# Kernel optimization log

Hardware: AMD Instinct MI355X
Metric: run time of the kernel (lower is better)

Reference implementation:

```python
import jax, jax.numpy as jnp
import numpy as np

LN_EPS = 1e-5

def setup_inputs() -> dict:
    num_nodes, embed_dim, bs, E = 10000, 64, 32, 200000
    key = jax.random.key(0)
    ks = jax.random.split(key, 8)
    d_in = 2 * embed_dim + 1  # msg_dim = 1
    d_h = 4 * embed_dim
    return {
        "users": jax.random.randint(ks[0], (E,), 0, num_nodes * bs),
        "items": jax.random.randint(ks[1], (E,), 0, num_nodes * bs),
        "messages": jax.random.normal(ks[2], (E,), dtype=jnp.float32),
        "bs": bs,
        "user_emb": jax.random.normal(ks[3], (num_nodes, embed_dim), dtype=jnp.float32) * 0.02,
        "item_emb": jax.random.normal(ks[4], (num_nodes, embed_dim), dtype=jnp.float32) * 0.02,
        "W1": jax.random.normal(ks[5], (d_in, d_h), dtype=jnp.float32) * 0.02,
        "b1": jnp.zeros((d_h,), dtype=jnp.float32),
        "ln_g": jnp.ones((d_h,), dtype=jnp.float32),
        "ln_b": jnp.zeros((d_h,), dtype=jnp.float32),
        "W2": jax.random.normal(ks[6], (d_h, d_h), dtype=jnp.float32) * 0.02,
        "b2": jnp.zeros((d_h,), dtype=jnp.float32),
    }

def reference(users, items, messages, bs, user_emb, item_emb, W1, b1, ln_g, ln_b, W2, b2):
    num_nodes, embed_dim = user_emb.shape
    N = num_nodes * bs
    msgs = messages.astype(jnp.float32).reshape(-1, 1)          # [E,1]
    ue = user_emb[users % num_nodes]                             # [E,D]
    ie = item_emb[items % num_nodes]                             # [E,D]
    x = jnp.concatenate([ue, ie, msgs], axis=-1)                 # [E,2D+1]
    h = x @ W1 + b1                                              # [E,4D]
    mu = jnp.mean(h, axis=-1, keepdims=True)
    var = jnp.mean(jnp.square(h - mu), axis=-1, keepdims=True)
    hn = (h - mu) * jax.lax.rsqrt(var + LN_EPS) * ln_g + ln_b
    enc = hn @ W2 + b2                                           # [E,4D]
    uu, iu, ug, ig = jnp.split(enc, 4, axis=-1)                  # each [E,D]
    user_state = jnp.zeros((N, embed_dim), jnp.float32).at[users].add(uu)
    item_state = jnp.zeros((N, embed_dim), jnp.float32).at[items].add(iu)
    user_global = jnp.zeros((N, embed_dim), jnp.float32).at[users].add(ug)
    item_global = jnp.zeros((N, embed_dim), jnp.float32).at[items].add(ig)
    # reshape (num_nodes, bs, D) -> (bs, num_nodes, D)
    up = jnp.transpose(user_global.reshape(num_nodes, bs, embed_dim), (1, 0, 2))
    ip = jnp.transpose(item_global.reshape(num_nodes, bs, embed_dim), (1, 0, 2))
    up = jnp.mean(up, axis=1, keepdims=True)                     # [bs,1,D]
    ip = jnp.mean(ip, axis=1, keepdims=True)
    ret_u = jnp.transpose(user_state.reshape(num_nodes, bs, embed_dim), (1, 0, 2)) + up
    ret_i = jnp.transpose(item_state.reshape(num_nodes, bs, embed_dim), (1, 0, 2)) + ip
    return (ret_u, ret_i)
```

## Files before the change

### kernel.cpp

```cpp
#include <hip/hip_runtime.h>
#include <hip/hip_bf16.h>


typedef __attribute__((ext_vector_type(8))) short bf8_t;
typedef __attribute__((ext_vector_type(4))) float f32x4;

union FragU { bf8_t f; unsigned int u[4]; };

static __device__ __forceinline__ unsigned short f2bf(float f) {
    unsigned int x = __float_as_uint(f);
    return (unsigned short)((x + 0x7fffu + ((x >> 16) & 1u)) >> 16);
}
#define B2F_LO(u) __uint_as_float((u) << 16)
#define B2F_HI(u) __uint_as_float((u) & 0xffff0000u)

__global__ void zero_f4_kernel(float4* p, int n4) {
    int i = blockIdx.x * 256 + threadIdx.x;
    int stride = gridDim.x * 256;
    float4 z = make_float4(0.f, 0.f, 0.f, 0.f);
    for (; i < n4; i += stride) p[i] = z;
}

__global__ void convert_kernel(const float* __restrict__ W1, const float* __restrict__ W2,
                               const float* __restrict__ uemb, const float* __restrict__ iemb,
                               unsigned short* __restrict__ w1f, unsigned short* __restrict__ w2f,
                               unsigned short* __restrict__ uembb, unsigned short* __restrict__ iembb,
                               int nemb4) {
    int idx = blockIdx.x * 256 + threadIdx.x;
    if (idx < 4096) {
        int l = idx & 63, fr = idx >> 6;
        int ks = fr & 3, nt = fr >> 2;
        int n = nt * 16 + (l & 15), g = l >> 4;
        unsigned short v[8];
#pragma unroll
        for (int e = 0; e < 8; e++) {
            int k = ks * 32 + ((e < 4) ? (4 * g + e) : (16 + 4 * g + (e - 4)));
            v[e] = f2bf(W1[k * 256 + n]);
        }
        uint4 pk;
        pk.x = (unsigned)v[0] | ((unsigned)v[1] << 16);
        pk.y = (unsigned)v[2] | ((unsigned)v[3] << 16);
        pk.z = (unsigned)v[4] | ((unsigned)v[5] << 16);
        pk.w = (unsigned)v[6] | ((unsigned)v[7] << 16);
        *(uint4*)&w1f[idx * 8] = pk;
    } else if (idx < 12288) {
        int t = idx - 4096;
        int l = t & 63, fr = t >> 6;
        int ks = fr & 7, nt = fr >> 3;
        int n = nt * 16 + (l & 15), g = l >> 4;
        unsigned short v[8];
#pragma unroll
        for (int e = 0; e < 8; e++) {
            int k = ks * 32 + ((e < 4) ? (4 * g + e) : (16 + 4 * g + (e - 4)));
            v[e] = f2bf(W2[k * 256 + n]);
        }
        uint4 pk;
        pk.x = (unsigned)v[0] | ((unsigned)v[1] << 16);
        pk.y = (unsigned)v[2] | ((unsigned)v[3] << 16);
        pk.z = (unsigned)v[4] | ((unsigned)v[5] << 16);
        pk.w = (unsigned)v[6] | ((unsigned)v[7] << 16);
        *(uint4*)&w2f[t * 8] = pk;
    }
    if (nemb4 > 0) {
        int total = gridDim.x * 256;
        for (int i = idx; i < 2 * nemb4; i += total) {
            int isU = (i < nemb4);
            int j = isU ? i : i - nemb4;
            float4 v = isU ? ((const float4*)uemb)[j] : ((const float4*)iemb)[j];
            ushort4 p;
            p.x = f2bf(v.x); p.y = f2bf(v.y); p.z = f2bf(v.z); p.w = f2bf(v.w);
            unsigned short* dst = isU ? uembb : iembb;
            *(ushort4*)&dst[(long)j * 4] = p;
        }
    }
}

__global__ __launch_bounds__(512, 2)
void encode_mfma_kernel(const int* __restrict__ users, const int* __restrict__ items,
                        const float* __restrict__ msgs,
                        const float* __restrict__ uemb, const float* __restrict__ iemb,
                        const unsigned short* __restrict__ uembb, const unsigned short* __restrict__ iembb,
                        const float* __restrict__ W1, const float* __restrict__ b1,
                        const float* __restrict__ ln_g, const float* __restrict__ ln_b,
                        const float* __restrict__ b2,
                        const unsigned short* __restrict__ w1f, const unsigned short* __restrict__ w2f,
                        float* __restrict__ out, float* __restrict__ glob,
                        int E, int num_nodes, int bs, long out_half, int usebf) {
    __shared__ __align__(16) unsigned short xhb[64 * 256];
    __shared__ __align__(16) float gacc[4096];
    __shared__ __align__(16) float msgs_s[64];
    __shared__ __align__(16) int ubase_s[64], ibase_s[64];

    const int tid = threadIdx.x;
    const int w = tid >> 6;
    const int l = tid & 63;
    const int g = l >> 4;
    const int m16 = l & 15;
    const int nnD = num_nodes * 64;

    for (int i = tid; i < 4096; i += 512) gacc[i] = 0.f;

    bf8_t w1frag[2][4], w2frag[2][8];
#pragma unroll
    for (int ntl = 0; ntl < 2; ntl++) {
        int nt = w * 2 + ntl;
#pragma unroll
        for (int ks = 0; ks < 4; ks++)
            w1frag[ntl][ks] = *(const bf8_t*)&w1f[((nt * 4 + ks) * 64 + l) * 8];
#pragma unroll
        for (int ks = 0; ks < 8; ks++)
            w2frag[ntl][ks] = *(const bf8_t*)&w2f[((nt * 8 + ks) * 64 + l) * 8];
    }

    float b1v[2], w128v[2], b2v[2];
#pragma unroll
    for (int ntl = 0; ntl < 2; ntl++) {
        int j = w * 32 + ntl * 16 + m16;
        b1v[ntl] = b1[j];
        w128v[ntl] = W1[128 * 256 + j];
        b2v[ntl] = b2[j];
    }
    float* outi = out + out_half;

    const int nTiles = (E + 63) >> 6;
    for (int tile = blockIdx.x; tile < nTiles; tile += gridDim.x) {
        const int e0 = tile << 6;
        __syncthreads();

        if (tid < 64) {
            int ev = e0 + tid;
            if (ev < E) {
                int u = users[ev], it = items[ev];
                int ub = u % bs, un = u / bs, ib = it % bs, in_ = it / bs;
                ubase_s[tid] = (ub * nnD + un * 64) | (ub << 26);
                ibase_s[tid] = (ib * nnD + in_ * 64) | (ib << 26);
                msgs_s[tid] = msgs[ev];
            } else {
                ubase_s[tid] = -1; ibase_s[tid] = -1; msgs_s[tid] = 0.f;
            }
        }
        for (int idx = tid; idx < 1024; idx += 512) {
            int e = idx >> 4, q = idx & 15;
            int ev = e0 + e;
            uint4 v = make_uint4(0u, 0u, 0u, 0u);
            if (ev < E) {
                if (usebf) {
                    if (q < 8) { int u = users[ev] % num_nodes; v = *(const uint4*)&uembb[(long)u * 64 + q * 8]; }
                    else       { int it = items[ev] % num_nodes; v = *(const uint4*)&iembb[(long)it * 64 + (q - 8) * 8]; }
                } else {
                    const float* src; long base;
                    if (q < 8) { int u = users[ev] % num_nodes; src = uemb; base = (long)u * 64 + q * 8; }
                    else       { int it = items[ev] % num_nodes; src = iemb; base = (long)it * 64 + (q - 8) * 8; }
                    float4 a0 = *(const float4*)&src[base];
                    float4 a1 = *(const float4*)&src[base + 4];
                    v.x = (unsigned)f2bf(a0.x) | ((unsigned)f2bf(a0.y) << 16);
                    v.y = (unsigned)f2bf(a0.z) | ((unsigned)f2bf(a0.w) << 16);
                    v.z = (unsigned)f2bf(a1.x) | ((unsigned)f2bf(a1.y) << 16);
                    v.w = (unsigned)f2bf(a1.z) | ((unsigned)f2bf(a1.w) << 16);
                }
            }
            int byte = (q * 16) ^ ((e & 7) << 4);
            *(uint4*)&xhb[e * 128 + (byte >> 1)] = v;
        }
        __syncthreads();

        f32x4 acc[4][2];
#pragma unroll
        for (int mt = 0; mt < 4; mt++) {
            const float* mgp = &msgs_s[mt * 16 + 4 * g];
            float mg[4] = {mgp[0], mgp[1], mgp[2], mgp[3]};
#pragma unroll
            for (int ntl = 0; ntl < 2; ntl++) {
                f32x4 a;
#pragma unroll
                for (int r = 0; r < 4; r++) a[r] = fmaf(mg[r], w128v[ntl], b1v[ntl]);
                acc[mt][ntl] = a;
            }
        }
#pragma unroll
        for (int ks = 0; ks < 4; ks++) {
            FragU a[4];
#pragma unroll
            for (int mt = 0; mt < 4; mt++) {
                int i = mt * 16 + m16;
                int bir0 = (ks * 64 + 8 * g) ^ ((i & 7) << 4);
                int bir1 = (ks * 64 + 32 + 8 * g) ^ ((i & 7) << 4);
                uint2 c0 = *(const uint2*)&xhb[i * 128 + (bir0 >> 1)];
                uint2 c1 = *(const uint2*)&xhb[i * 128 + (bir1 >> 1)];
                a[mt].u[0] = c0.x; a[mt].u[1] = c0.y; a[mt].u[2] = c1.x; a[mt].u[3] = c1.y;
            }
#pragma unroll
            for (int ntl = 0; ntl < 2; ntl++)
#pragma unroll
                for (int mt = 0; mt < 4; mt++)
                    acc[mt][ntl] = __builtin_amdgcn_mfma_f32_16x16x32_bf16(
                        a[mt].f, w1frag[ntl][ks], acc[mt][ntl], 0, 0, 0);
        }
        __syncthreads();

#pragma unroll
        for (int mt = 0; mt < 4; mt++)
#pragma unroll
            for (int ntl = 0; ntl < 2; ntl++)
#pragma unroll
                for (int r = 0; r < 4; r++) {
                    int e = mt * 16 + 4 * g + r;
                    int j = w * 32 + ntl * 16 + m16;
                    int byte = (2 * j) ^ ((e & 15) << 4);
                    xhb[e * 256 + (byte >> 1)] = f2bf(acc[mt][ntl][r]);
                }
        __syncthreads();

#pragma unroll
        for (int it = 0; it < 4; it++) {
            int e = w * 8 + it * 2 + (l >> 5);
            int slot = l & 31;
            int byte = (slot * 16) ^ ((e & 15) << 4);
            uint4 hv = *(const uint4*)&xhb[e * 256 + (byte >> 1)];
            float f0 = B2F_LO(hv.x), f1 = B2F_HI(hv.x);
            float f2 = B2F_LO(hv.y), f3 = B2F_HI(hv.y);
            float f4 = B2F_LO(hv.z), f5 = B2F_HI(hv.z);
            float f6 = B2F_LO(hv.w), f7 = B2F_HI(hv.w);
            float s1 = ((f0 + f1) + (f2 + f3)) + ((f4 + f5) + (f6 + f7));
            float s2 = ((f0*f0 + f1*f1) + (f2*f2 + f3*f3)) + ((f4*f4 + f5*f5) + (f6*f6 + f7*f7));
#pragma unroll
            for (int mk = 1; mk <= 16; mk <<= 1) {
                s1 += __shfl_xor(s1, mk);
                s2 += __shfl_xor(s2, mk);
            }
            float mu = s1 * (1.f / 256.f);
            float var = s2 * (1.f / 256.f) - mu * mu;
            float rs = rsqrtf(var + 1e-5f);
            int jb = (slot ^ (e & 15)) * 8;
            float4 g0 = *(const float4*)&ln_g[jb];
            float4 g1 = *(const float4*)&ln_g[jb + 4];
            float4 bb0 = *(const float4*)&ln_b[jb];
            float4 bb1 = *(const float4*)&ln_b[jb + 4];
            float n0 = fmaf((f0 - mu) * rs, g0.x, bb0.x);
            float n1 = fmaf((f1 - mu) * rs, g0.y, bb0.y);
            float n2 = fmaf((f2 - mu) * rs, g0.z, bb0.z);
            float n3 = fmaf((f3 - mu) * rs, g0.w, bb0.w);
            float n4 = fmaf((f4 - mu) * rs, g1.x, bb1.x);
            float n5 = fmaf((f5 - mu) * rs, g1.y, bb1.y);
            float n6 = fmaf((f6 - mu) * rs, g1.z, bb1.z);
            float n7 = fmaf((f7 - mu) * rs, g1.w, bb1.w);
            uint4 pv;
            pv.x = (unsigned)f2bf(n0) | ((unsigned)f2bf(n1) << 16);
            pv.y = (unsigned)f2bf(n2) | ((unsigned)f2bf(n3) << 16);
            pv.z = (unsigned)f2bf(n4) | ((unsigned)f2bf(n5) << 16);
            pv.w = (unsigned)f2bf(n6) | ((unsigned)f2bf(n7) << 16);
            *(uint4*)&xhb[e * 256 + (byte >> 1)] = pv;
        }
        __syncthreads();

#pragma unroll
        for (int mt = 0; mt < 4; mt++)
#pragma unroll
            for (int ntl = 0; ntl < 2; ntl++) {
                f32x4 a;
#pragma unroll
                for (int r = 0; r < 4; r++) a[r] = b2v[ntl];
                acc[mt][ntl] = a;
            }
#pragma unroll
        for (int ks = 0; ks < 8; ks++) {
            FragU a[4];
#pragma unroll
            for (int mt = 0; mt < 4; mt++) {
                int i = mt * 16 + m16;
                int bir0 = (ks * 64 + 8 * g) ^ ((i & 15) << 4);
                int bir1 = (ks * 64 + 32 + 8 * g) ^ ((i & 15) << 4);
                uint2 c0 = *(const uint2*)&xhb[i * 256 + (bir0 >> 1)];
                uint2 c1 = *(const uint2*)&xhb[i * 256 + (bir1 >> 1)];
                a[mt].u[0] = c0.x; a[mt].u[1] = c0.y; a[mt].u[2] = c1.x; a[mt].u[3] = c1.y;
            }
#pragma unroll
            for (int ntl = 0; ntl < 2; ntl++)
#pragma unroll
                for (int mt = 0; mt < 4; mt++)
                    acc[mt][ntl] = __builtin_amdgcn_mfma_f32_16x16x32_bf16(
                        a[mt].f, w2frag[ntl][ks], acc[mt][ntl], 0, 0, 0);
        }

        const int q = w >> 1;
        const int dbase = (w & 1) * 32;
        const int* barr = (q & 1) ? ibase_s : ubase_s;
#pragma unroll
        for (int mt = 0; mt < 4; mt++) {
            int4 bb = *(const int4*)&barr[mt * 16 + 4 * g];
            int bvv[4] = {bb.x, bb.y, bb.z, bb.w};
#pragma unroll
            for (int ntl = 0; ntl < 2; ntl++) {
                int d = dbase + ntl * 16 + m16;
#pragma unroll
                for (int r = 0; r < 4; r++) {
                    int v = bvv[r];
                    if (v >= 0) {
                        float val = acc[mt][ntl][r];
                        if (q == 0)      atomicAdd(&out[(v & 0x03FFFFFF) + d], val);
                        else if (q == 1) atomicAdd(&outi[(v & 0x03FFFFFF) + d], val);
                        else if (q == 2) atomicAdd(&gacc[(v >> 26) * 64 + d], val);
                        else             atomicAdd(&gacc[2048 + (v >> 26) * 64 + d], val);
                    }
                }
            }
        }
    }

    __syncthreads();
    for (int i = tid; i < 4096; i += 512) {
        float v = gacc[i];
        if (v != 0.f) atomicAdd(&glob[i], v);
    }
}

__global__ void finalize_kernel(float* __restrict__ out, const float* __restrict__ glob,
                                long out_half, long nnD, float inv_nodes, int n4) {
    int i4 = blockIdx.x * 256 + threadIdx.x;
    int stride = gridDim.x * 256;
    for (; i4 < n4; i4 += stride) {
        long i = (long)i4 * 4;
        int half = (i >= out_half) ? 1 : 0;
        long r = half ? (i - out_half) : i;
        int b = (int)(r / nnD);
        int dq = (int)(i & 63);
        float4 gv = *(const float4*)&glob[half * 2048 + b * 64 + dq];
        float4 o = ((float4*)out)[i4];
        o.x += gv.x * inv_nodes;
        o.y += gv.y * inv_nodes;
        o.z += gv.z * inv_nodes;
        o.w += gv.w * inv_nodes;
        ((float4*)out)[i4] = o;
    }
}

extern "C" void kernel_launch(void* const* d_in, const int* in_sizes, int n_in,
                              void* d_out, int out_size, void* d_ws, size_t ws_size,
                              hipStream_t stream) {
    const int* users = (const int*)d_in[0];
    const int* items = (const int*)d_in[1];
    const float* msgs = (const float*)d_in[2];
    const float* uemb = (const float*)d_in[4];
    const float* iemb = (const float*)d_in[5];
    const float* W1 = (const float*)d_in[6];
    const float* b1 = (const float*)d_in[7];
    const float* ln_g = (const float*)d_in[8];
    const float* ln_b = (const float*)d_in[9];
    const float* W2 = (const float*)d_in[10];
    const float* b2 = (const float*)d_in[11];

    const int E = in_sizes[0];
    const int dh = in_sizes[7];
    const int D = dh / 4;
    const int num_nodes = in_sizes[4] / D;
    const long out_half = (long)out_size / 2;
    const int bs = (int)(out_half / ((long)num_nodes * D));

    float* out = (float*)d_out;
    float* glob = (float*)d_ws;
    unsigned short* w1f = (unsigned short*)((char*)d_ws + 16384);
    unsigned short* w2f = (unsigned short*)((char*)d_ws + 16384 + 65536);
    size_t embb_off = 16384 + 65536 + 131072;
    size_t embb_bytes = (size_t)num_nodes * 64 * 2;
    int usebf = (ws_size >= embb_off + 2 * embb_bytes) ? 1 : 0;
    unsigned short* uembb = usebf ? (unsigned short*)((char*)d_ws + embb_off) : nullptr;
    unsigned short* iembb = usebf ? (unsigned short*)((char*)d_ws + embb_off + embb_bytes) : nullptr;
    int nemb4 = usebf ? (num_nodes * 16) : 0;

    zero_f4_kernel<<<2048, 256, 0, stream>>>((float4*)out, out_size / 4);
    zero_f4_kernel<<<4, 256, 0, stream>>>((float4*)glob, 4096 / 4);
    convert_kernel<<<256, 256, 0, stream>>>(W1, W2, uemb, iemb, w1f, w2f, uembb, iembb, nemb4);

    encode_mfma_kernel<<<512, 512, 0, stream>>>(
        users, items, msgs, uemb, iemb, uembb, iembb,
        W1, b1, ln_g, ln_b, b2, w1f, w2f, out, glob,
        E, num_nodes, bs, out_half, usebf);

    finalize_kernel<<<2048, 256, 0, stream>>>(out, glob, out_half,
                                              (long)num_nodes * 64, 1.0f / num_nodes,
                                              out_size / 4);
}
```

Baseline: 479.7 us.

## Scatter node states via packed bf16 atomics into node-major scratch buffers

Adds a path that writes the user/item state contributions into bf16 scratch buffers laid out node-major, using packed bf16x2 global atomics after staging the accumulators through shared memory. The finalize kernel then transposes to the output layout and adds the global means. This halves atomic traffic and improves locality of scatter writes. The cost is an extra shared-memory staging pass with barriers, a 2x larger zeroing pass over scratch, and bf16 rounding of the summed states, which may hurt accuracy. The path only runs when the workspace is large enough.

Measured after the change: 510.7 us. +6.5%, slower.

```diff
diff --git a/kernel.cpp b/kernel.cpp
--- a/kernel.cpp
+++ b/kernel.cpp
@@ -14,9 +14,27 @@
 #define B2F_LO(u) __uint_as_float((u) << 16)
 #define B2F_HI(u) __uint_as_float((u) & 0xffff0000u)
 
-__global__ void zero_f4_kernel(float4* p, int n4) {
-    int i = blockIdx.x * 256 + threadIdx.x;
-    int stride = gridDim.x * 256;
+template <typename T>
+static __device__ __forceinline__ auto pk_add_impl(T* p, T v, int)
+    -> decltype(unsafeAtomicAdd(p, v), void()) {
+    unsafeAtomicAdd(p, v);
+}
+template <typename T>
+static __device__ __forceinline__ void pk_add_impl(T* p, T v, long) {
+    unsigned int raw;
+    __builtin_memcpy(&raw, &v, 4);
+    asm volatile("global_atomic_pk_add_bf16 %0, %1, off\n\ts_waitcnt vmcnt(0)"
+                 :: "v"(p), "v"(raw) : "memory");
+}
+static __device__ __forceinline__ void pk_atomic_add(__hip_bfloat162* dst, unsigned int pkbits) {
+    __hip_bfloat162 v;
+    __builtin_memcpy(&v, &pkbits, 4);
+    pk_add_impl(dst, v, 0);
+}
+
+__global__ void zero_f4_kernel(float4* p, long n4) {
+    long i = (long)blockIdx.x * 256 + threadIdx.x;
+    long stride = (long)gridDim.x * 256;
     float4 z = make_float4(0.f, 0.f, 0.f, 0.f);
     for (; i < n4; i += stride) p[i] = z;
 }
@@ -75,6 +93,7 @@
     }
 }
 
+template<bool PK>
 __global__ __launch_bounds__(512, 2)
 void encode_mfma_kernel(const int* __restrict__ users, const int* __restrict__ items,
                         const float* __restrict__ msgs,
@@ -85,6 +104,7 @@
                         const float* __restrict__ b2,
                         const unsigned short* __restrict__ w1f, const unsigned short* __restrict__ w2f,
                         float* __restrict__ out, float* __restrict__ glob,
+                        unsigned short* __restrict__ uscr, unsigned short* __restrict__ iscr,
                         int E, int num_nodes, int bs, long out_half, int usebf) {
     __shared__ __align__(16) unsigned short xhb[64 * 256];
     __shared__ __align__(16) float gacc[4096];
@@ -121,6 +141,7 @@
         b2v[ntl] = b2[j];
     }
     float* outi = out + out_half;
+    float* f32s = (float*)xhb;
 
     const int nTiles = (E + 63) >> 6;
     for (int tile = blockIdx.x; tile < nTiles; tile += gridDim.x) {
@@ -131,9 +152,15 @@
             int ev = e0 + tid;
             if (ev < E) {
                 int u = users[ev], it = items[ev];
-                int ub = u % bs, un = u / bs, ib = it % bs, in_ = it / bs;
-                ubase_s[tid] = (ub * nnD + un * 64) | (ub << 26);
-                ibase_s[tid] = (ib * nnD + in_ * 64) | (ib << 26);
+                int ub = u % bs, ib = it % bs;
+                if (PK) {
+                    ubase_s[tid] = (u * 64) | (ub << 26);
+                    ibase_s[tid] = (it * 64) | (ib << 26);
+                } else {
+                    int un = u / bs, in_ = it / bs;
+                    ubase_s[tid] = (ub * nnD + un * 64) | (ub << 26);
+                    ibase_s[tid] = (ib * nnD + in_ * 64) | (ib << 26);
+                }
                 msgs_s[tid] = msgs[ev];
             } else {
                 ubase_s[tid] = -1; ibase_s[tid] = -1; msgs_s[tid] = 0.f;
@@ -282,25 +309,80 @@
                         a[mt].f, w2frag[ntl][ks], acc[mt][ntl], 0, 0, 0);
         }
 
-        const int q = w >> 1;
-        const int dbase = (w & 1) * 32;
-        const int* barr = (q & 1) ? ibase_s : ubase_s;
-#pragma unroll
-        for (int mt = 0; mt < 4; mt++) {
-            int4 bb = *(const int4*)&barr[mt * 16 + 4 * g];
-            int bvv[4] = {bb.x, bb.y, bb.z, bb.w};
-#pragma unroll
-            for (int ntl = 0; ntl < 2; ntl++) {
-                int d = dbase + ntl * 16 + m16;
-#pragma unroll
-                for (int r = 0; r < 4; r++) {
-                    int v = bvv[r];
-                    if (v >= 0) {
-                        float val = acc[mt][ntl][r];
-                        if (q == 0)      atomicAdd(&out[(v & 0x03FFFFFF) + d], val);
-                        else if (q == 1) atomicAdd(&outi[(v & 0x03FFFFFF) + d], val);
-                        else if (q == 2) atomicAdd(&gacc[(v >> 26) * 64 + d], val);
-                        else             atomicAdd(&gacc[2048 + (v >> 26) * 64 + d], val);
+        if (PK) {
+            __syncthreads();
+
+            if (w < 4) {
+#pragma unroll
+                for (int mt = 0; mt < 4; mt++)
+#pragma unroll
+                    for (int ntl = 0; ntl < 2; ntl++)
+#pragma unroll
+                        for (int r = 0; r < 4; r++) {
+                            int e = mt * 16 + 4 * g + r;
+                            int c = w * 32 + ntl * 16 + m16;
+                            f32s[e * 128 + (c ^ ((e & 7) << 2))] = acc[mt][ntl][r];
+                        }
+            } else {
+                const int qq = w >> 1;
+                const int dbase = (w & 1) * 32;
+                const int* barr = (qq & 1) ? ibase_s : ubase_s;
+#pragma unroll
+                for (int mt = 0; mt < 4; mt++) {
+                    int4 bb = *(const int4*)&barr[mt * 16 + 4 * g];
+                    int bvv[4] = {bb.x, bb.y, bb.z, bb.w};
+#pragma unroll
+                    for (int ntl = 0; ntl < 2; ntl++) {
+                        int d = dbase + ntl * 16 + m16;
+#pragma unroll
+                        for (int r = 0; r < 4; r++) {
+                            int v = bvv[r];
+                            if (v >= 0) {
+                                float val = acc[mt][ntl][r];
+                                if (qq == 2) atomicAdd(&gacc[(v >> 26) * 64 + d], val);
+                                else         atomicAdd(&gacc[2048 + (v >> 26) * 64 + d], val);
+                            }
+                        }
+                    }
+                }
+            }
+            __syncthreads();
+
+#pragma unroll
+            for (int s = 0; s < 8; s++) {
+                int p = s * 512 + tid;
+                int e = p >> 6, k = p & 63;
+                int half = k >> 5, dp = k & 31;
+                int vbase = half ? ibase_s[e] : ubase_s[e];
+                if (vbase >= 0) {
+                    int c = half * 64 + dp * 2;
+                    float2 v = *(float2*)&f32s[e * 128 + (c ^ ((e & 7) << 2))];
+                    unsigned int pkb = (unsigned)f2bf(v.x) | ((unsigned)f2bf(v.y) << 16);
+                    unsigned short* base = half ? iscr : uscr;
+                    pk_atomic_add((__hip_bfloat162*)(base + (vbase & 0x03FFFFFF) + dp * 2), pkb);
+                }
+            }
+        } else {
+            const int q = w >> 1;
+            const int dbase = (w & 1) * 32;
+            const int* barr = (q & 1) ? ibase_s : ubase_s;
+#pragma unroll
+            for (int mt = 0; mt < 4; mt++) {
+                int4 bb = *(const int4*)&barr[mt * 16 + 4 * g];
+                int bvv[4] = {bb.x, bb.y, bb.z, bb.w};
+#pragma unroll
+                for (int ntl = 0; ntl < 2; ntl++) {
+                    int d = dbase + ntl * 16 + m16;
+#pragma unroll
+                    for (int r = 0; r < 4; r++) {
+                        int v = bvv[r];
+                        if (v >= 0) {
+                            float val = acc[mt][ntl][r];
+                            if (q == 0)      atomicAdd(&out[(v & 0x03FFFFFF) + d], val);
+                            else if (q == 1) atomicAdd(&outi[(v & 0x03FFFFFF) + d], val);
+                            else if (q == 2) atomicAdd(&gacc[(v >> 26) * 64 + d], val);
+                            else             atomicAdd(&gacc[2048 + (v >> 26) * 64 + d], val);
+                        }
                     }
                 }
             }
@@ -311,6 +393,33 @@
     for (int i = tid; i < 4096; i += 512) {
         float v = gacc[i];
         if (v != 0.f) atomicAdd(&glob[i], v);
+    }
+}
+
+__global__ void finalize_pk_kernel(float* __restrict__ out,
+                                   const unsigned short* __restrict__ uscr,
+                                   const unsigned short* __restrict__ iscr,
+                                   const float* __restrict__ glob,
+                                   long out_half, long nnD, float inv_nodes, int bs, long n4) {
+    long i4 = (long)blockIdx.x * 256 + threadIdx.x;
+    long stride = (long)gridDim.x * 256;
+    for (; i4 < n4; i4 += stride) {
+        long i = i4 * 4;
+        int half = (i >= out_half) ? 1 : 0;
+        long r = half ? (i - out_half) : i;
+        int b = (int)(r / nnD);
+        long rem = r - (long)b * nnD;
+        int node = (int)(rem >> 6);
+        int dq = (int)(i & 63);
+        const unsigned short* s = (half ? iscr : uscr) + ((long)node * bs + b) * 64 + dq;
+        ushort4 sv = *(const ushort4*)s;
+        float4 gv = *(const float4*)&glob[half * 2048 + b * 64 + dq];
+        float4 o;
+        o.x = B2F_LO((unsigned)sv.x) + gv.x * inv_nodes;
+        o.y = B2F_LO((unsigned)sv.y) + gv.y * inv_nodes;
+        o.z = B2F_LO((unsigned)sv.z) + gv.z * inv_nodes;
+        o.w = B2F_LO((unsigned)sv.w) + gv.w * inv_nodes;
+        ((float4*)out)[i4] = o;
     }
 }
 
@@ -367,16 +476,32 @@
     unsigned short* iembb = usebf ? (unsigned short*)((char*)d_ws + embb_off + embb_bytes) : nullptr;
     int nemb4 = usebf ? (num_nodes * 16) : 0;
 
-    zero_f4_kernel<<<2048, 256, 0, stream>>>((float4*)out, out_size / 4);
+    size_t scr_off = embb_off + 2 * embb_bytes;
+    size_t scr_bytes = (size_t)num_nodes * bs * 64 * 2;
+    int pk = (usebf && ws_size >= scr_off + 2 * scr_bytes) ? 1 : 0;
+    unsigned short* uscr = pk ? (unsigned short*)((char*)d_ws + scr_off) : nullptr;
+    unsigned short* iscr = pk ? (unsigned short*)((char*)d_ws + scr_off + scr_bytes) : nullptr;
+
     zero_f4_kernel<<<4, 256, 0, stream>>>((float4*)glob, 4096 / 4);
     convert_kernel<<<256, 256, 0, stream>>>(W1, W2, uemb, iemb, w1f, w2f, uembb, iembb, nemb4);
 
-    encode_mfma_kernel<<<512, 512, 0, stream>>>(
-        users, items, msgs, uemb, iemb, uembb, iembb,
-        W1, b1, ln_g, ln_b, b2, w1f, w2f, out, glob,
-        E, num_nodes, bs, out_half, usebf);
-
-    finalize_kernel<<<2048, 256, 0, stream>>>(out, glob, out_half,
-                                              (long)num_nodes * 64, 1.0f / num_nodes,
-                                              out_size / 4);
-}
+    if (pk) {
+        zero_f4_kernel<<<2048, 256, 0, stream>>>((float4*)uscr, (long)(2 * scr_bytes) / 16);
+        encode_mfma_kernel<true><<<512, 512, 0, stream>>>(
+            users, items, msgs, uemb, iemb, uembb, iembb,
+            W1, b1, ln_g, ln_b, b2, w1f, w2f, out, glob, uscr, iscr,
+            E, num_nodes, bs, out_half, usebf);
+        finalize_pk_kernel<<<2048, 256, 0, stream>>>(out, uscr, iscr, glob, out_half,
+                                                     (long)num_nodes * 64, 1.0f / num_nodes,
+                                                     bs, (long)out_size / 4);
+    } else {
+        zero_f4_kernel<<<2048, 256, 0, stream>>>((float4*)out, (long)out_size / 4);
+        encode_mfma_kernel<false><<<512, 512, 0, stream>>>(
+            users, items, msgs, uemb, iemb, uembb, iembb,
+            W1, b1, ln_g, ln_b, b2, w1f, w2f, out, glob, nullptr, nullptr,
+            E, num_nodes, bs, out_half, usebf);
+        finalize_kernel<<<2048, 256, 0, stream>>>(out, glob, out_half,
+                                                  (long)num_nodes * 64, 1.0f / num_nodes,
+                                                  out_size / 4);
+    }
+}
```

## Replace scatter atomics with CSR gather of bf16 encoded rows

Applied to the files above, without the earlier changes.

Builds a CSR index (histogram, three-pass scan, fill) mapping each output row to its contributing events. The encoder then writes the user/item state columns as bf16 rows to a workspace buffer instead of atomically adding them into the output. A finalize kernel gathers and sums each row's events, adding the global mean, which removes the separate output zeroing pass and the global fp32 atomics. The encoder also prefetches the next tile's indices and embeddings. The cost is several extra launches, a random-access gather, and bf16 rounding of the encoded values before summation. The new path runs only when the workspace is large enough, otherwise the old kernels are used.

After: 539.9 us. 1.13x slower.

```diff
diff --git a/kernel.cpp b/kernel.cpp
--- a/kernel.cpp
+++ b/kernel.cpp
@@ -14,9 +14,9 @@
 #define B2F_LO(u) __uint_as_float((u) << 16)
 #define B2F_HI(u) __uint_as_float((u) & 0xffff0000u)
 
-__global__ void zero_f4_kernel(float4* p, int n4) {
-    int i = blockIdx.x * 256 + threadIdx.x;
-    int stride = gridDim.x * 256;
+__global__ void zero_f4_kernel(float4* p, long n4) {
+    long i = (long)blockIdx.x * 256 + threadIdx.x;
+    long stride = (long)gridDim.x * 256;
     float4 z = make_float4(0.f, 0.f, 0.f, 0.f);
     for (; i < n4; i += stride) p[i] = z;
 }
@@ -75,28 +75,94 @@
     }
 }
 
+__global__ void hist_kernel(const int* __restrict__ users, const int* __restrict__ items,
+                            int* __restrict__ cnt, int N, int E) {
+    int i = blockIdx.x * 256 + threadIdx.x;
+    int st = gridDim.x * 256;
+    for (; i < E; i += st) {
+        atomicAdd(&cnt[users[i]], 1);
+        atomicAdd(&cnt[N + items[i]], 1);
+    }
+}
+
+__global__ void scan1_kernel(const int* __restrict__ cnt, int* __restrict__ bsum, int n) {
+    __shared__ int s[512];
+    int i = blockIdx.x * 512 + threadIdx.x;
+    s[threadIdx.x] = (i < n) ? cnt[i] : 0;
+    __syncthreads();
+    for (int off = 256; off; off >>= 1) {
+        if (threadIdx.x < off) s[threadIdx.x] += s[threadIdx.x + off];
+        __syncthreads();
+    }
+    if (threadIdx.x == 0) bsum[blockIdx.x] = s[0];
+}
+
+__global__ void scan2_kernel(int* __restrict__ bsum, int nb) {
+    int carry = 0;
+    for (int base = 0; base < nb; base += 64) {
+        int i = base + (int)threadIdx.x;
+        int orig = (i < nb) ? bsum[i] : 0;
+        int v = orig;
+#pragma unroll
+        for (int off = 1; off < 64; off <<= 1) {
+            int t = __shfl_up(v, off);
+            if ((int)threadIdx.x >= off) v += t;
+        }
+        if (i < nb) bsum[i] = carry + (v - orig);
+        carry += __shfl(v, 63);
+    }
+}
+
+__global__ void scan3_kernel(int* __restrict__ cnt , const int* __restrict__ bsum,
+                             int* __restrict__ off, int n, int total) {
+    __shared__ int s[512];
+    int i = blockIdx.x * 512 + threadIdx.x;
+    int orig = (i < n) ? cnt[i] : 0;
+    s[threadIdx.x] = orig;
+    __syncthreads();
+    for (int o = 1; o < 512; o <<= 1) {
+        int t = (threadIdx.x >= (unsigned)o) ? s[threadIdx.x - o] : 0;
+        __syncthreads();
+        s[threadIdx.x] += t;
+        __syncthreads();
+    }
+    int excl = s[threadIdx.x] - orig + bsum[blockIdx.x];
+    if (i < n) { off[i] = excl; cnt[i] = excl; }
+    if (i == n - 1) off[n] = total;
+}
+
+__global__ void fill_kernel(const int* __restrict__ users, const int* __restrict__ items,
+                            int* __restrict__ cur, int* __restrict__ evid, int N, int E) {
+    int i = blockIdx.x * 256 + threadIdx.x;
+    int st = gridDim.x * 256;
+    for (; i < E; i += st) {
+        int p = atomicAdd(&cur[users[i]], 1);
+        evid[p] = i;
+        int q = atomicAdd(&cur[N + items[i]], 1);
+        evid[q] = i;
+    }
+}
+
 __global__ __launch_bounds__(512, 2)
-void encode_mfma_kernel(const int* __restrict__ users, const int* __restrict__ items,
-                        const float* __restrict__ msgs,
-                        const float* __restrict__ uemb, const float* __restrict__ iemb,
-                        const unsigned short* __restrict__ uembb, const unsigned short* __restrict__ iembb,
-                        const float* __restrict__ W1, const float* __restrict__ b1,
-                        const float* __restrict__ ln_g, const float* __restrict__ ln_b,
-                        const float* __restrict__ b2,
-                        const unsigned short* __restrict__ w1f, const unsigned short* __restrict__ w2f,
-                        float* __restrict__ out, float* __restrict__ glob,
-                        int E, int num_nodes, int bs, long out_half, int usebf) {
+void encode_csr_kernel(const int* __restrict__ users, const int* __restrict__ items,
+                       const float* __restrict__ msgs,
+                       const unsigned short* __restrict__ uembb, const unsigned short* __restrict__ iembb,
+                       const float* __restrict__ W1, const float* __restrict__ b1,
+                       const float* __restrict__ ln_g, const float* __restrict__ ln_b,
+                       const float* __restrict__ b2,
+                       const unsigned short* __restrict__ w1f, const unsigned short* __restrict__ w2f,
+                       unsigned short* __restrict__ enc, float* __restrict__ glob,
+                       int E, int num_nodes, int bs) {
     __shared__ __align__(16) unsigned short xhb[64 * 256];
     __shared__ __align__(16) float gacc[4096];
     __shared__ __align__(16) float msgs_s[64];
-    __shared__ __align__(16) int ubase_s[64], ibase_s[64];
+    __shared__ __align__(16) int ubb_s[64], ibb_s[64];
 
     const int tid = threadIdx.x;
     const int w = tid >> 6;
     const int l = tid & 63;
     const int g = l >> 4;
     const int m16 = l & 15;
-    const int nnD = num_nodes * 64;
 
     for (int i = tid; i < 4096; i += 512) gacc[i] = 0.f;
 
@@ -120,49 +186,57 @@
         w128v[ntl] = W1[128 * 256 + j];
         b2v[ntl] = b2[j];
     }
-    float* outi = out + out_half;
+    float* f32s = (float*)xhb;
+
+    const int ce = tid >> 4;
+    const int cq = tid & 15;
+    int praw[2];
+    int pu = -1, pi = -1; float pmsg = 0.f;
+    uint4 pemb[2];
 
     const int nTiles = (E + 63) >> 6;
-    for (int tile = blockIdx.x; tile < nTiles; tile += gridDim.x) {
+    const int tstep = gridDim.x;
+
+    auto prefetch_idx = [&](int e0p) {
+#pragma unroll
+        for (int c = 0; c < 2; c++) {
+            int ev = e0p + ce + 32 * c;
+            praw[c] = (ev < E) ? ((cq < 8) ? users[ev] : items[ev]) : 0;
+        }
+        if (tid < 64) {
+            int ev = e0p + tid;
+            if (ev < E) { pu = users[ev]; pi = items[ev]; pmsg = msgs[ev]; }
+            else        { pu = -1; pi = -1; pmsg = 0.f; }
+        }
+    };
+    auto prefetch_emb = [&]() {
+#pragma unroll
+        for (int c = 0; c < 2; c++) {
+            int row = praw[c] % num_nodes;
+            const unsigned short* t = (cq < 8) ? uembb : iembb;
+            pemb[c] = *(const uint4*)&t[(long)row * 64 + (cq & 7) * 8];
+        }
+    };
+
+    if (blockIdx.x < nTiles) { prefetch_idx(blockIdx.x << 6); prefetch_emb(); }
+
+    for (int tile = blockIdx.x; tile < nTiles; tile += tstep) {
         const int e0 = tile << 6;
         __syncthreads();
 
         if (tid < 64) {
-            int ev = e0 + tid;
-            if (ev < E) {
-                int u = users[ev], it = items[ev];
-                int ub = u % bs, un = u / bs, ib = it % bs, in_ = it / bs;
-                ubase_s[tid] = (ub * nnD + un * 64) | (ub << 26);
-                ibase_s[tid] = (ib * nnD + in_ * 64) | (ib << 26);
-                msgs_s[tid] = msgs[ev];
-            } else {
-                ubase_s[tid] = -1; ibase_s[tid] = -1; msgs_s[tid] = 0.f;
-            }
-        }
-        for (int idx = tid; idx < 1024; idx += 512) {
-            int e = idx >> 4, q = idx & 15;
-            int ev = e0 + e;
-            uint4 v = make_uint4(0u, 0u, 0u, 0u);
-            if (ev < E) {
-                if (usebf) {
-                    if (q < 8) { int u = users[ev] % num_nodes; v = *(const uint4*)&uembb[(long)u * 64 + q * 8]; }
-                    else       { int it = items[ev] % num_nodes; v = *(const uint4*)&iembb[(long)it * 64 + (q - 8) * 8]; }
-                } else {
-                    const float* src; long base;
-                    if (q < 8) { int u = users[ev] % num_nodes; src = uemb; base = (long)u * 64 + q * 8; }
-                    else       { int it = items[ev] % num_nodes; src = iemb; base = (long)it * 64 + (q - 8) * 8; }
-                    float4 a0 = *(const float4*)&src[base];
-                    float4 a1 = *(const float4*)&src[base + 4];
-                    v.x = (unsigned)f2bf(a0.x) | ((unsigned)f2bf(a0.y) << 16);
-                    v.y = (unsigned)f2bf(a0.z) | ((unsigned)f2bf(a0.w) << 16);
-                    v.z = (unsigned)f2bf(a1.x) | ((unsigned)f2bf(a1.y) << 16);
-                    v.w = (unsigned)f2bf(a1.z) | ((unsigned)f2bf(a1.w) << 16);
-                }
-            }
-            int byte = (q * 16) ^ ((e & 7) << 4);
-            *(uint4*)&xhb[e * 128 + (byte >> 1)] = v;
-        }
-        __syncthreads();
+            if (pu >= 0) { ubb_s[tid] = pu % bs; ibb_s[tid] = pi % bs; msgs_s[tid] = pmsg; }
+            else         { ubb_s[tid] = -1; ibb_s[tid] = -1; msgs_s[tid] = 0.f; }
+        }
+#pragma unroll
+        for (int c = 0; c < 2; c++) {
+            int e = ce + 32 * c;
+            int byte = (cq * 16) ^ ((e & 7) << 4);
+            *(uint4*)&xhb[e * 128 + (byte >> 1)] = pemb[c];
+        }
+        __syncthreads();
+
+        prefetch_idx((tile + tstep) << 6);
 
         f32x4 acc[4][2];
 #pragma unroll
@@ -210,6 +284,8 @@
                     xhb[e * 256 + (byte >> 1)] = f2bf(acc[mt][ntl][r]);
                 }
         __syncthreads();
+
+        prefetch_emb();
 
 #pragma unroll
         for (int it = 0; it < 4; it++) {
@@ -281,6 +357,313 @@
                     acc[mt][ntl] = __builtin_amdgcn_mfma_f32_16x16x32_bf16(
                         a[mt].f, w2frag[ntl][ks], acc[mt][ntl], 0, 0, 0);
         }
+        __syncthreads();
+
+        if (w < 4) {
+#pragma unroll
+            for (int mt = 0; mt < 4; mt++)
+#pragma unroll
+                for (int ntl = 0; ntl < 2; ntl++)
+#pragma unroll
+                    for (int r = 0; r < 4; r++) {
+                        int e = mt * 16 + 4 * g + r;
+                        int c = w * 32 + ntl * 16 + m16;
+                        f32s[e * 128 + (c ^ ((e & 7) << 2))] = acc[mt][ntl][r];
+                    }
+        } else {
+            const int qq = w >> 1;
+            const int dbase = (w & 1) * 32;
+            const int* barr = (qq & 1) ? ibb_s : ubb_s;
+#pragma unroll
+            for (int mt = 0; mt < 4; mt++) {
+                int4 bb = *(const int4*)&barr[mt * 16 + 4 * g];
+                int bvv[4] = {bb.x, bb.y, bb.z, bb.w};
+#pragma unroll
+                for (int ntl = 0; ntl < 2; ntl++) {
+                    int d = dbase + ntl * 16 + m16;
+#pragma unroll
+                    for (int r = 0; r < 4; r++) {
+                        int b = bvv[r];
+                        if (b >= 0) {
+                            float val = acc[mt][ntl][r];
+                            if (qq == 2) atomicAdd(&gacc[b * 64 + d], val);
+                            else         atomicAdd(&gacc[2048 + b * 64 + d], val);
+                        }
+                    }
+                }
+            }
+        }
+        __syncthreads();
+
+        {
+            int e = tid >> 3, sub = tid & 7;
+            int swz = (e & 7) << 2;
+            const float* rowp = &f32s[e * 128];
+            float4 a0 = *(const float4*)&rowp[(sub * 16 + 0) ^ swz];
+            float4 a1 = *(const float4*)&rowp[(sub * 16 + 4) ^ swz];
+            float4 a2 = *(const float4*)&rowp[(sub * 16 + 8) ^ swz];
+            float4 a3 = *(const float4*)&rowp[(sub * 16 + 12) ^ swz];
+            uint4 o0, o1;
+            o0.x = (unsigned)f2bf(a0.x) | ((unsigned)f2bf(a0.y) << 16);
+            o0.y = (unsigned)f2bf(a0.z) | ((unsigned)f2bf(a0.w) << 16);
+            o0.z = (unsigned)f2bf(a1.x) | ((unsigned)f2bf(a1.y) << 16);
+            o0.w = (unsigned)f2bf(a1.z) | ((unsigned)f2bf(a1.w) << 16);
+            o1.x = (unsigned)f2bf(a2.x) | ((unsigned)f2bf(a2.y) << 16);
+            o1.y = (unsigned)f2bf(a2.z) | ((unsigned)f2bf(a2.w) << 16);
+            o1.z = (unsigned)f2bf(a3.x) | ((unsigned)f2bf(a3.y) << 16);
+            o1.w = (unsigned)f2bf(a3.z) | ((unsigned)f2bf(a3.w) << 16);
+            unsigned short* ep = enc + (size_t)(e0 + e) * 128 + sub * 16;
+            *(uint4*)&ep[0] = o0;
+            *(uint4*)&ep[8] = o1;
+        }
+    }
+
+    __syncthreads();
+    for (int i = tid; i < 4096; i += 512) {
+        float v = gacc[i];
+        if (v != 0.f) atomicAdd(&glob[i], v);
+    }
+}
+
+__global__ void finalize_gather_kernel(float* __restrict__ out,
+                                       const int* __restrict__ off, const int* __restrict__ evid,
+                                       const unsigned short* __restrict__ enc,
+                                       const float* __restrict__ glob,
+                                       long out_half, int nnD, float inv_nodes,
+                                       int bs, int N, long n4) {
+    long i4 = (long)blockIdx.x * 256 + threadIdx.x;
+    long stride = (long)gridDim.x * 256;
+    for (; i4 < n4; i4 += stride) {
+        long i = i4 * 4;
+        int half = (i >= out_half) ? 1 : 0;
+        long r = half ? (i - out_half) : i;
+        int b = (int)(r / nnD);
+        int rem = (int)(r - (long)b * nnD);
+        int node = rem >> 6;
+        int dq = rem & 63;
+        int row = node * bs + b;
+        int idx = half ? (N + row) : row;
+        int s0 = off[idx], s1 = off[idx + 1];
+        float4 gv = *(const float4*)&glob[half * 2048 + b * 64 + dq];
+        float4 acc = make_float4(gv.x * inv_nodes, gv.y * inv_nodes,
+                                 gv.z * inv_nodes, gv.w * inv_nodes);
+        int colb = half * 64 + dq;
+        for (int s = s0; s < s1; s++) {
+            int ev = evid[s];
+            uint2 p = *(const uint2*)&enc[(size_t)ev * 128 + colb];
+            acc.x += B2F_LO(p.x); acc.y += B2F_HI(p.x);
+            acc.z += B2F_LO(p.y); acc.w += B2F_HI(p.y);
+        }
+        ((float4*)out)[i4] = acc;
+    }
+}
+
+__global__ __launch_bounds__(512, 2)
+void encode_mfma_kernel(const int* __restrict__ users, const int* __restrict__ items,
+                        const float* __restrict__ msgs,
+                        const float* __restrict__ uemb, const float* __restrict__ iemb,
+                        const unsigned short* __restrict__ uembb, const unsigned short* __restrict__ iembb,
+                        const float* __restrict__ W1, const float* __restrict__ b1,
+                        const float* __restrict__ ln_g, const float* __restrict__ ln_b,
+                        const float* __restrict__ b2,
+                        const unsigned short* __restrict__ w1f, const unsigned short* __restrict__ w2f,
+                        float* __restrict__ out, float* __restrict__ glob,
+                        int E, int num_nodes, int bs, long out_half, int usebf) {
+    __shared__ __align__(16) unsigned short xhb[64 * 256];
+    __shared__ __align__(16) float gacc[4096];
+    __shared__ __align__(16) float msgs_s[64];
+    __shared__ __align__(16) int ubase_s[64], ibase_s[64];
+
+    const int tid = threadIdx.x;
+    const int w = tid >> 6;
+    const int l = tid & 63;
+    const int g = l >> 4;
+    const int m16 = l & 15;
+    const int nnD = num_nodes * 64;
+
+    for (int i = tid; i < 4096; i += 512) gacc[i] = 0.f;
+
+    bf8_t w1frag[2][4], w2frag[2][8];
+#pragma unroll
+    for (int ntl = 0; ntl < 2; ntl++) {
+        int nt = w * 2 + ntl;
+#pragma unroll
+        for (int ks = 0; ks < 4; ks++)
+            w1frag[ntl][ks] = *(const bf8_t*)&w1f[((nt * 4 + ks) * 64 + l) * 8];
+#pragma unroll
+        for (int ks = 0; ks < 8; ks++)
+            w2frag[ntl][ks] = *(const bf8_t*)&w2f[((nt * 8 + ks) * 64 + l) * 8];
+    }
+
+    float b1v[2], w128v[2], b2v[2];
+#pragma unroll
+    for (int ntl = 0; ntl < 2; ntl++) {
+        int j = w * 32 + ntl * 16 + m16;
+        b1v[ntl] = b1[j];
+        w128v[ntl] = W1[128 * 256 + j];
+        b2v[ntl] = b2[j];
+    }
+    float* outi = out + out_half;
+
+    const int nTiles = (E + 63) >> 6;
+    for (int tile = blockIdx.x; tile < nTiles; tile += gridDim.x) {
+        const int e0 = tile << 6;
+        __syncthreads();
+
+        if (tid < 64) {
+            int ev = e0 + tid;
+            if (ev < E) {
+                int u = users[ev], it = items[ev];
+                int ub = u % bs, un = u / bs, ib = it % bs, in_ = it / bs;
+                ubase_s[tid] = (ub * nnD + un * 64) | (ub << 26);
+                ibase_s[tid] = (ib * nnD + in_ * 64) | (ib << 26);
+                msgs_s[tid] = msgs[ev];
+            } else {
+                ubase_s[tid] = -1; ibase_s[tid] = -1; msgs_s[tid] = 0.f;
+            }
+        }
+        for (int idx = tid; idx < 1024; idx += 512) {
+            int e = idx >> 4, q = idx & 15;
+            int ev = e0 + e;
+            uint4 v = make_uint4(0u, 0u, 0u, 0u);
+            if (ev < E) {
+                if (usebf) {
+                    if (q < 8) { int u = users[ev] % num_nodes; v = *(const uint4*)&uembb[(long)u * 64 + q * 8]; }
+                    else       { int it = items[ev] % num_nodes; v = *(const uint4*)&iembb[(long)it * 64 + (q - 8) * 8]; }
+                } else {
+                    const float* src; long base;
+                    if (q < 8) { int u = users[ev] % num_nodes; src = uemb; base = (long)u * 64 + q * 8; }
+                    else       { int it = items[ev] % num_nodes; src = iemb; base = (long)it * 64 + (q - 8) * 8; }
+                    float4 a0 = *(const float4*)&src[base];
+                    float4 a1 = *(const float4*)&src[base + 4];
+                    v.x = (unsigned)f2bf(a0.x) | ((unsigned)f2bf(a0.y) << 16);
+                    v.y = (unsigned)f2bf(a0.z) | ((unsigned)f2bf(a0.w) << 16);
+                    v.z = (unsigned)f2bf(a1.x) | ((unsigned)f2bf(a1.y) << 16);
+                    v.w = (unsigned)f2bf(a1.z) | ((unsigned)f2bf(a1.w) << 16);
+                }
+            }
+            int byte = (q * 16) ^ ((e & 7) << 4);
+            *(uint4*)&xhb[e * 128 + (byte >> 1)] = v;
+        }
+        __syncthreads();
+
+        f32x4 acc[4][2];
+#pragma unroll
+        for (int mt = 0; mt < 4; mt++) {
+            const float* mgp = &msgs_s[mt * 16 + 4 * g];
+            float mg[4] = {mgp[0], mgp[1], mgp[2], mgp[3]};
+#pragma unroll
+            for (int ntl = 0; ntl < 2; ntl++) {
+                f32x4 a;
+#pragma unroll
+                for (int r = 0; r < 4; r++) a[r] = fmaf(mg[r], w128v[ntl], b1v[ntl]);
+                acc[mt][ntl] = a;
+            }
+        }
+#pragma unroll
+        for (int ks = 0; ks < 4; ks++) {
+            FragU a[4];
+#pragma unroll
+            for (int mt = 0; mt < 4; mt++) {
+                int i = mt * 16 + m16;
+                int bir0 = (ks * 64 + 8 * g) ^ ((i & 7) << 4);
+                int bir1 = (ks * 64 + 32 + 8 * g) ^ ((i & 7) << 4);
+                uint2 c0 = *(const uint2*)&xhb[i * 128 + (bir0 >> 1)];
+                uint2 c1 = *(const uint2*)&xhb[i * 128 + (bir1 >> 1)];
+                a[mt].u[0] = c0.x; a[mt].u[1] = c0.y; a[mt].u[2] = c1.x; a[mt].u[3] = c1.y;
+            }
+#pragma unroll
+            for (int ntl = 0; ntl < 2; ntl++)
+#pragma unroll
+                for (int mt = 0; mt < 4; mt++)
+                    acc[mt][ntl] = __builtin_amdgcn_mfma_f32_16x16x32_bf16(
+                        a[mt].f, w1frag[ntl][ks], acc[mt][ntl], 0, 0, 0);
+        }
+        __syncthreads();
+
+#pragma unroll
+        for (int mt = 0; mt < 4; mt++)
+#pragma unroll
+            for (int ntl = 0; ntl < 2; ntl++)
+#pragma unroll
+                for (int r = 0; r < 4; r++) {
+                    int e = mt * 16 + 4 * g + r;
+                    int j = w * 32 + ntl * 16 + m16;
+                    int byte = (2 * j) ^ ((e & 15) << 4);
+                    xhb[e * 256 + (byte >> 1)] = f2bf(acc[mt][ntl][r]);
+                }
+        __syncthreads();
+
+#pragma unroll
+        for (int it = 0; it < 4; it++) {
+            int e = w * 8 + it * 2 + (l >> 5);
+            int slot = l & 31;
+            int byte = (slot * 16) ^ ((e & 15) << 4);
+            uint4 hv = *(const uint4*)&xhb[e * 256 + (byte >> 1)];
+            float f0 = B2F_LO(hv.x), f1 = B2F_HI(hv.x);
+            float f2 = B2F_LO(hv.y), f3 = B2F_HI(hv.y);
+            float f4 = B2F_LO(hv.z), f5 = B2F_HI(hv.z);
+            float f6 = B2F_LO(hv.w), f7 = B2F_HI(hv.w);
+            float s1 = ((f0 + f1) + (f2 + f3)) + ((f4 + f5) + (f6 + f7));
+            float s2 = ((f0*f0 + f1*f1) + (f2*f2 + f3*f3)) + ((f4*f4 + f5*f5) + (f6*f6 + f7*f7));
+#pragma unroll
+            for (int mk = 1; mk <= 16; mk <<= 1) {
+                s1 += __shfl_xor(s1, mk);
+                s2 += __shfl_xor(s2, mk);
+            }
+            float mu = s1 * (1.f / 256.f);
+            float var = s2 * (1.f / 256.f) - mu * mu;
+            float rs = rsqrtf(var + 1e-5f);
+            int jb = (slot ^ (e & 15)) * 8;
+            float4 g0 = *(const float4*)&ln_g[jb];
+            float4 g1 = *(const float4*)&ln_g[jb + 4];
+            float4 bb0 = *(const float4*)&ln_b[jb];
+            float4 bb1 = *(const float4*)&ln_b[jb + 4];
+            float n0 = fmaf((f0 - mu) * rs, g0.x, bb0.x);
+            float n1 = fmaf((f1 - mu) * rs, g0.y, bb0.y);
+            float n2 = fmaf((f2 - mu) * rs, g0.z, bb0.z);
+            float n3 = fmaf((f3 - mu) * rs, g0.w, bb0.w);
+            float n4 = fmaf((f4 - mu) * rs, g1.x, bb1.x);
+            float n5 = fmaf((f5 - mu) * rs, g1.y, bb1.y);
+            float n6 = fmaf((f6 - mu) * rs, g1.z, bb1.z);
+            float n7 = fmaf((f7 - mu) * rs, g1.w, bb1.w);
+            uint4 pv;
+            pv.x = (unsigned)f2bf(n0) | ((unsigned)f2bf(n1) << 16);
+            pv.y = (unsigned)f2bf(n2) | ((unsigned)f2bf(n3) << 16);
+            pv.z = (unsigned)f2bf(n4) | ((unsigned)f2bf(n5) << 16);
+            pv.w = (unsigned)f2bf(n6) | ((unsigned)f2bf(n7) << 16);
+            *(uint4*)&xhb[e * 256 + (byte >> 1)] = pv;
+        }
+        __syncthreads();
+
+#pragma unroll
+        for (int mt = 0; mt < 4; mt++)
+#pragma unroll
+            for (int ntl = 0; ntl < 2; ntl++) {
+                f32x4 a;
+#pragma unroll
+                for (int r = 0; r < 4; r++) a[r] = b2v[ntl];
+                acc[mt][ntl] = a;
+            }
+#pragma unroll
+        for (int ks = 0; ks < 8; ks++) {
+            FragU a[4];
+#pragma unroll
+            for (int mt = 0; mt < 4; mt++) {
+                int i = mt * 16 + m16;
+                int bir0 = (ks * 64 + 8 * g) ^ ((i & 15) << 4);
+                int bir1 = (ks * 64 + 32 + 8 * g) ^ ((i & 15) << 4);
+                uint2 c0 = *(const uint2*)&xhb[i * 256 + (bir0 >> 1)];
+                uint2 c1 = *(const uint2*)&xhb[i * 256 + (bir1 >> 1)];
+                a[mt].u[0] = c0.x; a[mt].u[1] = c0.y; a[mt].u[2] = c1.x; a[mt].u[3] = c1.y;
+            }
+#pragma unroll
+            for (int ntl = 0; ntl < 2; ntl++)
+#pragma unroll
+                for (int mt = 0; mt < 4; mt++)
+                    acc[mt][ntl] = __builtin_amdgcn_mfma_f32_16x16x32_bf16(
+                        a[mt].f, w2frag[ntl][ks], acc[mt][ntl], 0, 0, 0);
+        }
 
         const int q = w >> 1;
         const int dbase = (w & 1) * 32;
@@ -355,28 +738,69 @@
     const int num_nodes = in_sizes[4] / D;
     const long out_half = (long)out_size / 2;
     const int bs = (int)(out_half / ((long)num_nodes * D));
+    const int N = num_nodes * bs;
+    const int nnD = num_nodes * 64;
 
     float* out = (float*)d_out;
     float* glob = (float*)d_ws;
     unsigned short* w1f = (unsigned short*)((char*)d_ws + 16384);
-    unsigned short* w2f = (unsigned short*)((char*)d_ws + 16384 + 65536);
-    size_t embb_off = 16384 + 65536 + 131072;
+    unsigned short* w2f = (unsigned short*)((char*)d_ws + 81920);
     size_t embb_bytes = (size_t)num_nodes * 64 * 2;
-    int usebf = (ws_size >= embb_off + 2 * embb_bytes) ? 1 : 0;
-    unsigned short* uembb = usebf ? (unsigned short*)((char*)d_ws + embb_off) : nullptr;
-    unsigned short* iembb = usebf ? (unsigned short*)((char*)d_ws + embb_off + embb_bytes) : nullptr;
+    size_t uembb_off = 212992;
+    size_t iembb_off = uembb_off + embb_bytes;
+    size_t need_bf = iembb_off + embb_bytes;
+    int usebf = (ws_size >= need_bf) ? 1 : 0;
+    unsigned short* uembb = usebf ? (unsigned short*)((char*)d_ws + uembb_off) : nullptr;
+    unsigned short* iembb = usebf ? (unsigned short*)((char*)d_ws + iembb_off) : nullptr;
     int nemb4 = usebf ? (num_nodes * 16) : 0;
 
-    zero_f4_kernel<<<2048, 256, 0, stream>>>((float4*)out, out_size / 4);
+    size_t cnt_off  = (need_bf + 255) & ~(size_t)255;
+    size_t off_off  = cnt_off + (size_t)2 * N * 4;
+    off_off = (off_off + 255) & ~(size_t)255;
+    size_t bsum_off = off_off + ((size_t)2 * N + 1) * 4;
+    bsum_off = (bsum_off + 255) & ~(size_t)255;
+    int nb = (2 * N + 511) / 512;
+    size_t evid_off = bsum_off + (size_t)nb * 4;
+    evid_off = (evid_off + 255) & ~(size_t)255;
+    size_t enc_off  = evid_off + (size_t)2 * E * 4;
+    enc_off = (enc_off + 255) & ~(size_t)255;
+    int EP = (E + 63) & ~63;
+    size_t need_csr = enc_off + (size_t)EP * 256;
+    int csr = (usebf && ws_size >= need_csr) ? 1 : 0;
+
     zero_f4_kernel<<<4, 256, 0, stream>>>((float4*)glob, 4096 / 4);
     convert_kernel<<<256, 256, 0, stream>>>(W1, W2, uemb, iemb, w1f, w2f, uembb, iembb, nemb4);
 
-    encode_mfma_kernel<<<512, 512, 0, stream>>>(
-        users, items, msgs, uemb, iemb, uembb, iembb,
-        W1, b1, ln_g, ln_b, b2, w1f, w2f, out, glob,
-        E, num_nodes, bs, out_half, usebf);
-
-    finalize_kernel<<<2048, 256, 0, stream>>>(out, glob, out_half,
-                                              (long)num_nodes * 64, 1.0f / num_nodes,
-                                              out_size / 4);
-}
+    if (csr) {
+        int* cnt  = (int*)((char*)d_ws + cnt_off);
+        int* offp = (int*)((char*)d_ws + off_off);
+        int* bsum = (int*)((char*)d_ws + bsum_off);
+        int* evid = (int*)((char*)d_ws + evid_off);
+        unsigned short* enc = (unsigned short*)((char*)d_ws + enc_off);
+
+        zero_f4_kernel<<<512, 256, 0, stream>>>((float4*)cnt, ((long)2 * N * 4) / 16);
+        hist_kernel<<<512, 256, 0, stream>>>(users, items, cnt, N, E);
+        scan1_kernel<<<nb, 512, 0, stream>>>(cnt, bsum, 2 * N);
+        scan2_kernel<<<1, 64, 0, stream>>>(bsum, nb);
+        scan3_kernel<<<nb, 512, 0, stream>>>(cnt, bsum, offp, 2 * N, 2 * E);
+        fill_kernel<<<512, 256, 0, stream>>>(users, items, cnt, evid, N, E);
+
+        encode_csr_kernel<<<512, 512, 0, stream>>>(
+            users, items, msgs, uembb, iembb,
+            W1, b1, ln_g, ln_b, b2, w1f, w2f, enc, glob,
+            E, num_nodes, bs);
+
+        finalize_gather_kernel<<<2048, 256, 0, stream>>>(
+            out, offp, evid, enc, glob, out_half, nnD,
+            1.0f / num_nodes, bs, N, (long)out_size / 4);
+    } else {
+        zero_f4_kernel<<<2048, 256, 0, stream>>>((float4*)out, (long)out_size / 4);
+        encode_mfma_kernel<<<512, 512, 0, stream>>>(
+            users, items, msgs, uemb, iemb, uembb, iembb,
+            W1, b1, ln_g, ln_b, b2, w1f, w2f, out, glob,
+            E, num_nodes, bs, out_half, usebf);
+        finalize_kernel<<<2048, 256, 0, stream>>>(out, glob, out_half,
+                                                  (long)nnD, 1.0f / num_nodes,
+                                                  out_size / 4);
+    }
+}
```
